# Performance work log

Measured on AMD Instinct MI355X. Metric: run time of the kernel, lower is better.

## Reference

```python
import jax, jax.numpy as jnp
import numpy as np

N = 50000   # nodes
E = 200000  # edges
C = 32      # conv_dim
ND = 75     # n_atom_features
ED = 12     # n_bond_features
L = 3       # num_layer
G = 500     # num graphs in batch
HID = 5     # neurons_message
EPS = 1e-5


def leaky(v):
    return jnp.where(v > 0, v, 0.01 * v)


def setup_inputs() -> dict:
    key = jax.random.key(0)
    ks = jax.random.split(key, 16)
    x = jax.random.normal(ks[0], (N, ND), jnp.float32)
    edge_index = jax.random.randint(ks[1], (2, E), 0, N, jnp.int32)
    edge_attr = jax.random.uniform(ks[2], (E, ED), jnp.float32)
    batch = jnp.sort(jax.random.randint(ks[3], (N,), 0, G, jnp.int32))
    return {
        "x": x,
        "edge_index": edge_index,
        "edge_attr": edge_attr,
        "batch": batch,
        "lin_W": jax.random.normal(ks[4], (ND, C), jnp.float32) * 0.1,
        "lin_b": jnp.zeros((C,), jnp.float32),
        "mes_W1": jax.random.normal(ks[5], (L, ED, HID), jnp.float32) * 0.3,
        "mes_b1": jnp.zeros((L, HID), jnp.float32),
        "mes_W2": jax.random.normal(ks[6], (L, HID, C * C), jnp.float32) * 0.05,
        "mes_b2": jnp.zeros((L, C * C), jnp.float32),
        "root_W": jax.random.normal(ks[7], (L, C, C), jnp.float32) * 0.1,
        "conv_b": jnp.zeros((L, C), jnp.float32),
        "bn_g": jnp.ones((L, C), jnp.float32),
        "bn_b": jnp.zeros((L, C), jnp.float32),
        "pred_W": jax.random.normal(ks[8], (C, 1), jnp.float32) * 0.1,
        "pred_b": jnp.zeros((1,), jnp.float32),
    }


def reference(x, edge_index, edge_attr, batch, lin_W, lin_b, mes_W1, mes_b1,
              mes_W2, mes_b2, root_W, conv_b, bn_g, bn_b, pred_W, pred_b):
    src, dst = edge_index[0], edge_index[1]
    # initial atom projection
    h = leaky(x @ lin_W + lin_b)  # [N, C]
    for l in range(L):
        # edge MLP -> per-edge weight matrix [E, C, C]
        w = jnp.maximum(edge_attr @ mes_W1[l] + mes_b1[l], 0.0)
        w = (w @ mes_W2[l] + mes_b2[l]).reshape(E, C, C)
        # gather source features, per-edge matmul, scatter-add to targets
        msg = jnp.einsum('ec,ecd->ed', h[src], w)  # [E, C]
        agg = jax.ops.segment_sum(msg, dst, num_segments=N)  # [N, C]
        out = agg + h @ root_W[l] + conv_b[l]
        # batch norm (batch statistics over nodes)
        mu = out.mean(axis=0)
        var = out.var(axis=0)
        out = (out - mu) / jnp.sqrt(var + EPS) * bn_g[l] + bn_b[l]
        if l < L - 1:
            out = leaky(out)
        h = out  # JK == 'last'
    # graph readout: scatter_add over batch ids, then prediction head
    g = jax.ops.segment_sum(h, batch, num_segments=G)  # [G, C]
    return g @ pred_W + pred_b  # [G, 1]
```

## Files before the change

kernel.cpp:

```cpp
#include <hip/hip_runtime.h>

namespace {

constexpr int kN = 50000, kE = 200000, kG = 500;
constexpr float kEps = 1e-5f;
constexpr int kNB = (kN + 255) / 256;

typedef short v8s __attribute__((ext_vector_type(8)));
typedef float v4f __attribute__((ext_vector_type(4)));

__device__ __forceinline__ unsigned short bf16rn(float x) {
    unsigned u = __float_as_uint(x);
    return (unsigned short)((u + 0x7FFFu + ((u >> 16) & 1u)) >> 16);
}
__device__ __forceinline__ float bf16lo(unsigned p) { return __uint_as_float(p << 16); }
__device__ __forceinline__ float bf16hi(unsigned p) { return __uint_as_float(p & 0xFFFF0000u); }
__device__ __forceinline__ unsigned pk2(float a, float b) {
    return (unsigned)bf16rn(a) | ((unsigned)bf16rn(b) << 16);
}

__global__ __launch_bounds__(256) void zero_init(int* __restrict__ deg,
                                                 float* __restrict__ stats) {
    int i = blockIdx.x * 256 + threadIdx.x;
    if (i < kN) deg[i] = 0;
    if (i < 1536) stats[i] = 0.f;
}

__global__ __launch_bounds__(256) void deg_hist(
    const int* __restrict__ ei, int* __restrict__ deg)
{
    int e = blockIdx.x * 256 + threadIdx.x;
    if (e < kE) atomicAdd(&deg[ei[kE + e]], 1);
}

__global__ __launch_bounds__(1024) void init_h(
    const float* __restrict__ x, const float* __restrict__ W,
    const float* __restrict__ b, float* __restrict__ hbuf)
{
    __shared__ unsigned short sx[256 * 96];
    __shared__ unsigned short sW[32 * 96];
    int t = threadIdx.x;
    for (int i = t; i < 256 * 96; i += 1024) sx[i] = 0;
    for (int i = t; i < 32 * 96; i += 1024) sW[i] = 0;
    __syncthreads();
    int tb = blockIdx.x * 256;
    int cnt = min(256, kN - tb);
    for (int i = t; i < cnt * 75; i += 1024) {
        int n = i / 75, f = i - n * 75;
        sx[n * 96 + f] = bf16rn(x[(size_t)tb * 75 + i]);
    }
    for (int i = t; i < 75 * 32; i += 1024) {
        int f = i >> 5, c = i & 31;
        sW[c * 96 + f] = bf16rn(W[i]);
    }
    __syncthreads();
    int l15 = t & 15, quad = (t >> 4) & 3, w = t >> 6;
    #pragma unroll
    for (int tile = 0; tile < 2; ++tile) {
        v4f acc = {0.f, 0.f, 0.f, 0.f};
        #pragma unroll
        for (int kc = 0; kc < 3; ++kc) {
            v8s a  = *(const v8s*)&sx[(w * 16 + l15) * 96 + kc * 32 + quad * 8];
            v8s bb = *(const v8s*)&sW[(tile * 16 + l15) * 96 + kc * 32 + quad * 8];
            acc = __builtin_amdgcn_mfma_f32_16x16x32_bf16(a, bb, acc, 0, 0, 0);
        }
        int c = tile * 16 + l15;
        float bc = b[c];
        #pragma unroll
        for (int r = 0; r < 4; ++r) {
            int n = tb + w * 16 + quad * 4 + r;
            if (n < kN) {
                float v = acc[r] + bc;
                hbuf[(size_t)n * 32 + c] = v > 0.f ? v : 0.01f * v;
            }
        }
    }
}

__global__ __launch_bounds__(256) void scan_part(
    const int* __restrict__ deg, int* __restrict__ blkSum)
{
    __shared__ int sc[256];
    int t = threadIdx.x;
    int idx = blockIdx.x * 256 + t;
    sc[t] = (idx < kN) ? deg[idx] : 0;
    __syncthreads();
    #pragma unroll
    for (int off = 128; off > 0; off >>= 1) {
        if (t < off) sc[t] += sc[t + off];
        __syncthreads();
    }
    if (t == 0) blkSum[blockIdx.x] = sc[0];
}

__global__ __launch_bounds__(256) void scan_top(
    const int* __restrict__ blkSum, int* __restrict__ blkOff,
    int* __restrict__ rowptr)
{
    __shared__ int sc[256];
    int t = threadIdx.x;
    int v = (t < kNB) ? blkSum[t] : 0;
    sc[t] = v;
    __syncthreads();
    #pragma unroll
    for (int off = 1; off < 256; off <<= 1) {
        int u = (t >= off) ? sc[t - off] : 0;
        __syncthreads();
        sc[t] += u;
        __syncthreads();
    }
    if (t < kNB) blkOff[t] = sc[t] - v;
    if (t == kNB - 1) rowptr[kN] = sc[t];
}

__global__ __launch_bounds__(256) void scan_add(
    const int* __restrict__ deg, const int* __restrict__ blkOff,
    int* __restrict__ rowptr, int* __restrict__ cursor)
{
    __shared__ int sc[256];
    int t = threadIdx.x;
    int idx = blockIdx.x * 256 + t;
    int v = (idx < kN) ? deg[idx] : 0;
    sc[t] = v;
    __syncthreads();
    #pragma unroll
    for (int off = 1; off < 256; off <<= 1) {
        int u = (t >= off) ? sc[t - off] : 0;
        __syncthreads();
        sc[t] += u;
        __syncthreads();
    }
    if (idx < kN) {
        int p = blkOff[blockIdx.x] + sc[t] - v;
        rowptr[idx] = p;
        cursor[idx] = p;
    }
}

__global__ __launch_bounds__(256) void hid_pre(
    const float* __restrict__ ea, const float* __restrict__ W1,
    const float* __restrict__ b1, const int* __restrict__ ei,
    int* __restrict__ cursor, uint4* __restrict__ hcsr)
{
    __shared__ float sE[256 * 13];
    __shared__ float sW[195];
    int t = threadIdx.x;
    for (int i = t; i < 195; i += 256) sW[i] = (i < 180) ? W1[i] : b1[i - 180];
    int base = blockIdx.x * 256;
    int cnt = min(256, kE - base);
    for (int i = t; i < cnt * 12; i += 256) {
        int el = i / 12, f = i - el * 12;
        sE[el * 13 + f] = ea[(size_t)base * 12 + i];
    }
    __syncthreads();
    if (t >= cnt) return;
    int e = base + t;
    int src = ei[e];
    int dst = ei[kE + e];
    int pos = atomicAdd(&cursor[dst], 1);
    float ef[12];
    #pragma unroll
    for (int j = 0; j < 12; ++j) ef[j] = sE[t * 13 + j];
    #pragma unroll
    for (int l = 0; l < 3; ++l) {
        float h[5];
        #pragma unroll
        for (int k = 0; k < 5; ++k) h[k] = sW[180 + l * 5 + k];
        #pragma unroll
        for (int f = 0; f < 12; ++f)
            #pragma unroll
            for (int k = 0; k < 5; ++k)
                h[k] = fmaf(ef[f], sW[l * 60 + f * 5 + k], h[k]);
        #pragma unroll
        for (int k = 0; k < 5; ++k) h[k] = h[k] > 0.f ? h[k] : 0.f;
        hcsr[(size_t)l * kE + pos] =
            make_uint4(pk2(h[0], h[1]), pk2(h[2], h[3]), pk2(h[4], 0.f),
                       (unsigned)src);
    }
}

__global__ __launch_bounds__(1024) void y_root(
    const float* __restrict__ hbuf, float* __restrict__ obuf,
    const float* __restrict__ W2, const float* __restrict__ b2,
    const float* __restrict__ rW, const float* __restrict__ convb,
    const float* __restrict__ statsR,
    const float* __restrict__ gPrev, const float* __restrict__ bPrev,
    int first, unsigned* __restrict__ Ydw)
{
    __shared__ unsigned short sh[256 * 32];
    __shared__ unsigned short sB[256 * 32];
    int t = threadIdx.x;
    int tb = blockIdx.x * 256;
    int cnt = min(256, kN - tb);
    for (int i = t; i < 8192; i += 1024) {
        int co = i >> 5, c = i & 31, d = co >> 3, k = co & 7;
        float v = (k < 5) ? W2[k * 1024 + c * 32 + d]
                : (k == 5) ? b2[c * 32 + d]
                : (k == 6) ? rW[c * 32 + d] : 0.f;
        sB[co * 32 + c] = bf16rn(v);
    }
    if (first) {
        #pragma unroll
        for (int j = 0; j < 8; ++j) {
            int idx = t + j * 1024;
            int nl = idx >> 5, c = idx & 31;
            float v = (nl < cnt) ? hbuf[(size_t)(tb + nl) * 32 + c] : 0.f;
            sh[idx] = bf16rn(v);
        }
    } else {
        int c = t & 31;
        float sum = 0.f, sq = 0.f;
        #pragma unroll
        for (int r = 0; r < 8; ++r) {
            sum += statsR[r * 64 + c];
            sq  += statsR[r * 64 + 32 + c];
        }
        float mu = sum * (1.f / kN);
        float var = sq * (1.f / kN) - mu * mu;
        float ivg = rsqrtf(var + kEps) * gPrev[c];
        float bb = bPrev[c];
        #pragma unroll
        for (int j = 0; j < 8; ++j) {
            int idx = t + j * 1024;
            int nl = idx >> 5;
            float v = 0.f;
            if (nl < cnt) {
                float o = obuf[(size_t)(tb + nl) * 32 + c];
                v = (o - mu) * ivg + bb;
                v = v > 0.f ? v : 0.01f * v;
            }
            sh[idx] = bf16rn(v);
        }
    }
    __syncthreads();
    int l15 = t & 15, quad = (t >> 4) & 3, w = t >> 6;
    int n = tb + w * 16 + l15;
    v8s bn_ = *(const v8s*)&sh[(w * 16 + l15) * 32 + quad * 8];
    #pragma unroll
    for (int i = 0; i < 16; ++i) {
        v8s a = *(const v8s*)&sB[(i * 16 + l15) * 32 + quad * 8];
        v4f acc = {0.f, 0.f, 0.f, 0.f};
        acc = __builtin_amdgcn_mfma_f32_16x16x32_bf16(a, bn_, acc, 0, 0, 0);
        if (n < kN) {
            int cb = i * 16 + quad * 4;
            int d = cb >> 3, koff = cb & 7;
            if (koff == 0) {
                Ydw[(size_t)n * 128 + d * 4]     = pk2(acc[0], acc[1]);
                Ydw[(size_t)n * 128 + d * 4 + 1] = pk2(acc[2], acc[3]);
            } else {
                Ydw[(size_t)n * 128 + d * 4 + 2] = pk2(acc[0], acc[1]);
                obuf[(size_t)n * 32 + d] = acc[2] + convb[d];
            }
        }
    }
}

__global__ __launch_bounds__(256) void agg(
    const int* __restrict__ rowptr, const uint4* __restrict__ hcsr,
    const unsigned short* __restrict__ Yus, float* __restrict__ obuf,
    float* __restrict__ statsR)
{
    int t = threadIdx.x;
    int grp = t >> 5, d = t & 31;
    int nbase = blockIdx.x * 16 + grp * 2;
    float s = 0.f, q = 0.f;
    #pragma unroll
    for (int ii = 0; ii < 2; ++ii) {
        int n = nbase + ii;
        if (n < kN) {
            float acc = obuf[(size_t)n * 32 + d];
            int j0 = rowptr[n], j1 = rowptr[n + 1];
            for (int j = j0; j < j1; ++j) {
                uint4 hq = hcsr[j];
                uint4 p = *(const uint4*)(Yus + (size_t)hq.w * 256 + d * 8);
                float m = bf16hi(p.z);
                m = fmaf(bf16lo(hq.x), bf16lo(p.x), m);
                m = fmaf(bf16hi(hq.x), bf16hi(p.x), m);
                m = fmaf(bf16lo(hq.y), bf16lo(p.y), m);
                m = fmaf(bf16hi(hq.y), bf16hi(p.y), m);
                m = fmaf(bf16lo(hq.z), bf16lo(p.z), m);
                acc += m;
            }
            obuf[(size_t)n * 32 + d] = acc;
            s += acc; q += acc * acc;
        }
    }
    __shared__ float ls[256];
    __shared__ float lq[256];
    ls[t] = s; lq[t] = q;
    __syncthreads();
    if (t < 128) { ls[t] += ls[t + 128]; lq[t] += lq[t + 128]; }
    __syncthreads();
    if (t < 64) { ls[t] += ls[t + 64]; lq[t] += lq[t + 64]; }
    __syncthreads();
    if (t < 32) {
        float* rep = statsR + (blockIdx.x & 7) * 64;
        atomicAdd(&rep[t], ls[t] + ls[t + 32]);
        atomicAdd(&rep[32 + t], lq[t] + lq[t + 32]);
    }
}

__global__ __launch_bounds__(256) void bn_norm_final(
    const float* __restrict__ obuf, const float* __restrict__ statsR,
    const float* __restrict__ g, const float* __restrict__ b,
    float* __restrict__ vbuf, const float* __restrict__ predW,
    float* __restrict__ out, const float* __restrict__ pred_b)
{
    int idx = blockIdx.x * 256 + threadIdx.x;
    if (idx < kG) out[idx] = pred_b[0];
    if (idx >= kN * 32) return;
    int c = idx & 31;
    float sum = 0.f, sq = 0.f;
    #pragma unroll
    for (int r = 0; r < 8; ++r) {
        sum += statsR[r * 64 + c];
        sq  += statsR[r * 64 + 32 + c];
    }
    float mu = sum * (1.f / kN);
    float var = sq * (1.f / kN) - mu * mu;
    float inv = rsqrtf(var + kEps);
    float v = (obuf[idx] - mu) * inv * g[c] + b[c];
    float pv = v * predW[c];
    #pragma unroll
    for (int off = 16; off > 0; off >>= 1) pv += __shfl_down(pv, off, 32);
    if (c == 0) vbuf[idx >> 5] = pv;
}

__global__ __launch_bounds__(256) void seg_readout(
    const float* __restrict__ vbuf, const int* __restrict__ batch,
    float* __restrict__ out)
{
    __shared__ float ls[kG];
    int t = threadIdx.x;
    for (int i = t; i < kG; i += 256) ls[i] = 0.f;
    __syncthreads();
    int base = blockIdx.x * 2048 + t * 8;
    int cur = -1; float acc = 0.f;
    #pragma unroll
    for (int i = 0; i < 8; ++i) {
        int n = base + i;
        if (n >= kN) break;
        int gi = batch[n];
        float val = vbuf[n];
        if (gi != cur) {
            if (cur >= 0) atomicAdd(&ls[cur], acc);
            cur = gi; acc = val;
        } else acc += val;
    }
    if (cur >= 0) atomicAdd(&ls[cur], acc);
    __syncthreads();
    for (int i = t; i < kG; i += 256) {
        float s = ls[i];
        if (s != 0.f) atomicAdd(&out[i], s);
    }
}

}

extern "C" void kernel_launch(void* const* d_in, const int* in_sizes, int n_in,
                              void* d_out, int out_size, void* d_ws, size_t ws_size,
                              hipStream_t stream)
{
    const float* x      = (const float*)d_in[0];
    const int*   ei     = (const int*)d_in[1];
    const float* ea     = (const float*)d_in[2];
    const int*   batch  = (const int*)d_in[3];
    const float* lin_W  = (const float*)d_in[4];
    const float* lin_b  = (const float*)d_in[5];
    const float* mes_W1 = (const float*)d_in[6];
    const float* mes_b1 = (const float*)d_in[7];
    const float* mes_W2 = (const float*)d_in[8];
    const float* mes_b2 = (const float*)d_in[9];
    const float* root_W = (const float*)d_in[10];
    const float* conv_b = (const float*)d_in[11];
    const float* bn_g   = (const float*)d_in[12];
    const float* bn_b   = (const float*)d_in[13];
    const float* pred_W = (const float*)d_in[14];
    const float* pred_b = (const float*)d_in[15];
    float* out = (float*)d_out;

    char* wsb = (char*)d_ws;
    float* stats   = (float*)wsb;
    int* deg       = (int*)(wsb + 8192);
    int* rowptr    = deg + kN;
    int* cursor    = rowptr + kN + 1;
    int* blkSum    = cursor + kN;
    int* blkOff    = blkSum + 256;
    float* hbuf    = (float*)(blkOff + 256);
    float* obuf    = hbuf + (size_t)kN * 32;
    unsigned short* Yus = (unsigned short*)(obuf + (size_t)kN * 32);
    unsigned* Ydw  = (unsigned*)Yus;
    uint4* hcsr    = (uint4*)(Yus + (size_t)kN * 256);
    float* vbuf    = (float*)Yus;

    zero_init<<<kNB, 256, 0, stream>>>(deg, stats);
    deg_hist<<<(kE + 255) / 256, 256, 0, stream>>>(ei, deg);
    init_h<<<kNB, 1024, 0, stream>>>(x, lin_W, lin_b, hbuf);
    scan_part<<<kNB, 256, 0, stream>>>(deg, blkSum);
    scan_top<<<1, 256, 0, stream>>>(blkSum, blkOff, rowptr);
    scan_add<<<kNB, 256, 0, stream>>>(deg, blkOff, rowptr, cursor);
    hid_pre<<<(kE + 255) / 256, 256, 0, stream>>>(ea, mes_W1, mes_b1, ei,
                                                  cursor, hcsr);

    for (int l = 0; l < 3; ++l) {
        y_root<<<kNB, 1024, 0, stream>>>(
            hbuf, obuf, mes_W2 + (size_t)l * 5120, mes_b2 + (size_t)l * 1024,
            root_W + (size_t)l * 1024, conv_b + l * 32,
            stats + (l ? (l - 1) * 512 : 0),
            bn_g + (l ? (l - 1) * 32 : 0), bn_b + (l ? (l - 1) * 32 : 0),
            l == 0 ? 1 : 0, Ydw);
        agg<<<(kN + 15) / 16, 256, 0, stream>>>(
            rowptr, hcsr + (size_t)l * kE, Yus, obuf, stats + l * 512);
    }

    bn_norm_final<<<(kN * 32 + 255) / 256, 256, 0, stream>>>(
        obuf, stats + 2 * 512, bn_g + 64, bn_b + 64, vbuf, pred_W, out, pred_b);
    seg_readout<<<(kN + 2047) / 2048, 256, 0, stream>>>(vbuf, batch, out);
}
```

Baseline: 306.3 us.

## Replace node-centric CSR aggregation with edge-parallel segmented atomic scatter plus BN reduce

Node-parallel CSR gather aggregation is replaced by an edge-parallel kernel. Each 32-lane group handles 16 dst-sorted edges, combines runs with the same destination and flushes them with float atomics into obuf. Batch-norm statistics now come from a separate reduction kernel, and rowptr is no longer built. The source index is packed into 16 bits next to h[4], which only holds if node ids stay below 65536. The change aims to fix load imbalance from variable node degree, at the cost of atomics, an extra pass over obuf, and nondeterministic summation order.

```diff
diff --git a/kernel.cpp b/kernel.cpp
--- a/kernel.cpp
+++ b/kernel.cpp
@@ -5,6 +5,7 @@
 constexpr int kN = 50000, kE = 200000, kG = 500;
 constexpr float kEps = 1e-5f;
 constexpr int kNB = (kN + 255) / 256;
+constexpr int kEB = (kE + 255) / 256;
 
 typedef short v8s __attribute__((ext_vector_type(8)));
 typedef float v4f __attribute__((ext_vector_type(4)));
@@ -94,8 +95,7 @@
 }
 
 __global__ __launch_bounds__(256) void scan_top(
-    const int* __restrict__ blkSum, int* __restrict__ blkOff,
-    int* __restrict__ rowptr)
+    const int* __restrict__ blkSum, int* __restrict__ blkOff)
 {
     __shared__ int sc[256];
     int t = threadIdx.x;
@@ -110,12 +110,11 @@
         __syncthreads();
     }
     if (t < kNB) blkOff[t] = sc[t] - v;
-    if (t == kNB - 1) rowptr[kN] = sc[t];
 }
 
 __global__ __launch_bounds__(256) void scan_add(
     const int* __restrict__ deg, const int* __restrict__ blkOff,
-    int* __restrict__ rowptr, int* __restrict__ cursor)
+    int* __restrict__ cursor)
 {
     __shared__ int sc[256];
     int t = threadIdx.x;
@@ -130,17 +129,13 @@
         sc[t] += u;
         __syncthreads();
     }
-    if (idx < kN) {
-        int p = blkOff[blockIdx.x] + sc[t] - v;
-        rowptr[idx] = p;
-        cursor[idx] = p;
-    }
+    if (idx < kN) cursor[idx] = blkOff[blockIdx.x] + sc[t] - v;
 }
 
 __global__ __launch_bounds__(256) void hid_pre(
     const float* __restrict__ ea, const float* __restrict__ W1,
     const float* __restrict__ b1, const int* __restrict__ ei,
-    int* __restrict__ cursor, uint4* __restrict__ hcsr)
+    int* __restrict__ cursor, uint4* __restrict__ hq)
 {
     __shared__ float sE[256 * 13];
     __shared__ float sW[195];
@@ -155,8 +150,8 @@
     __syncthreads();
     if (t >= cnt) return;
     int e = base + t;
-    int src = ei[e];
-    int dst = ei[kE + e];
+    unsigned src = (unsigned)ei[e];
+    unsigned dst = (unsigned)ei[kE + e];
     int pos = atomicAdd(&cursor[dst], 1);
     float ef[12];
     #pragma unroll
@@ -173,9 +168,9 @@
                 h[k] = fmaf(ef[f], sW[l * 60 + f * 5 + k], h[k]);
         #pragma unroll
         for (int k = 0; k < 5; ++k) h[k] = h[k] > 0.f ? h[k] : 0.f;
-        hcsr[(size_t)l * kE + pos] =
-            make_uint4(pk2(h[0], h[1]), pk2(h[2], h[3]), pk2(h[4], 0.f),
-                       (unsigned)src);
+        hq[(size_t)l * kE + pos] = make_uint4(
+            pk2(h[0], h[1]), pk2(h[2], h[3]),
+            (unsigned)bf16rn(h[4]) | (src << 16), dst);
     }
 }
 
@@ -255,38 +250,48 @@
     }
 }
 
-__global__ __launch_bounds__(256) void agg(
-    const int* __restrict__ rowptr, const uint4* __restrict__ hcsr,
-    const unsigned short* __restrict__ Yus, float* __restrict__ obuf,
-    float* __restrict__ statsR)
-{
-    int t = threadIdx.x;
-    int grp = t >> 5, d = t & 31;
-    int nbase = blockIdx.x * 16 + grp * 2;
-    float s = 0.f, q = 0.f;
-    #pragma unroll
-    for (int ii = 0; ii < 2; ++ii) {
-        int n = nbase + ii;
-        if (n < kN) {
-            float acc = obuf[(size_t)n * 32 + d];
-            int j0 = rowptr[n], j1 = rowptr[n + 1];
-            for (int j = j0; j < j1; ++j) {
-                uint4 hq = hcsr[j];
-                uint4 p = *(const uint4*)(Yus + (size_t)hq.w * 256 + d * 8);
-                float m = bf16hi(p.z);
-                m = fmaf(bf16lo(hq.x), bf16lo(p.x), m);
-                m = fmaf(bf16hi(hq.x), bf16hi(p.x), m);
-                m = fmaf(bf16lo(hq.y), bf16lo(p.y), m);
-                m = fmaf(bf16hi(hq.y), bf16hi(p.y), m);
-                m = fmaf(bf16lo(hq.z), bf16lo(p.z), m);
-                acc += m;
-            }
-            obuf[(size_t)n * 32 + d] = acc;
-            s += acc; q += acc * acc;
-        }
-    }
+__global__ __launch_bounds__(256) void edge_scat(
+    const uint4* __restrict__ hq, const unsigned short* __restrict__ Yus,
+    float* __restrict__ obuf)
+{
+    int gid = blockIdx.x * 256 + threadIdx.x;
+    int grp = gid >> 5;
+    if (grp >= kE / 16) return;
+    int d = gid & 31;
+    int e0 = grp * 16;
+    float acc = 0.f;
+    unsigned cur = 0xFFFFFFFFu;
+    #pragma unroll 4
+    for (int i = 0; i < 16; ++i) {
+        uint4 q = hq[e0 + i];
+        unsigned src = q.z >> 16;
+        uint4 p = *(const uint4*)(Yus + (size_t)src * 256 + d * 8);
+        float m = bf16hi(p.z);
+        m = fmaf(bf16lo(q.x), bf16lo(p.x), m);
+        m = fmaf(bf16hi(q.x), bf16hi(p.x), m);
+        m = fmaf(bf16lo(q.y), bf16lo(p.y), m);
+        m = fmaf(bf16hi(q.y), bf16hi(p.y), m);
+        m = fmaf(bf16lo(q.z), bf16lo(p.z), m);
+        if (q.w != cur) {
+            if (cur != 0xFFFFFFFFu) atomicAdd(&obuf[(size_t)cur * 32 + d], acc);
+            cur = q.w; acc = m;
+        } else acc += m;
+    }
+    if (cur != 0xFFFFFFFFu) atomicAdd(&obuf[(size_t)cur * 32 + d], acc);
+}
+
+__global__ __launch_bounds__(256) void bn_reduce(
+    const float* __restrict__ obuf, float* __restrict__ statsR)
+{
     __shared__ float ls[256];
     __shared__ float lq[256];
+    int t = threadIdx.x;
+    int c = t & 31, row = t >> 5;
+    float s = 0.f, q = 0.f;
+    for (int n = blockIdx.x * 8 + row; n < kN; n += gridDim.x * 8) {
+        float v = obuf[(size_t)n * 32 + c];
+        s += v; q += v * v;
+    }
     ls[t] = s; lq[t] = q;
     __syncthreads();
     if (t < 128) { ls[t] += ls[t + 128]; lq[t] += lq[t + 128]; }
@@ -380,28 +385,27 @@
     float* out = (float*)d_out;
 
     char* wsb = (char*)d_ws;
-    float* stats   = (float*)wsb;
-    int* deg       = (int*)(wsb + 8192);
-    int* rowptr    = deg + kN;
-    int* cursor    = rowptr + kN + 1;
-    int* blkSum    = cursor + kN;
-    int* blkOff    = blkSum + 256;
-    float* hbuf    = (float*)(blkOff + 256);
-    float* obuf    = hbuf + (size_t)kN * 32;
+    float* stats = (float*)wsb;
+    int* deg     = (int*)(wsb + 8192);
+    int* cursor  = deg + kN;
+    int* blkSum  = cursor + kN;
+    int* blkOff  = blkSum + 256;
+    float* hbuf  = (float*)(blkOff + 256);
+    float* obuf  = hbuf + (size_t)kN * 32;
     unsigned short* Yus = (unsigned short*)(obuf + (size_t)kN * 32);
-    unsigned* Ydw  = (unsigned*)Yus;
-    uint4* hcsr    = (uint4*)(Yus + (size_t)kN * 256);
-    float* vbuf    = (float*)Yus;
+    unsigned* Ydw = (unsigned*)Yus;
+    uint4* hq    = (uint4*)(Yus + (size_t)kN * 256);
+    float* vbuf  = (float*)Yus;
 
     zero_init<<<kNB, 256, 0, stream>>>(deg, stats);
-    deg_hist<<<(kE + 255) / 256, 256, 0, stream>>>(ei, deg);
+    deg_hist<<<kEB, 256, 0, stream>>>(ei, deg);
     init_h<<<kNB, 1024, 0, stream>>>(x, lin_W, lin_b, hbuf);
     scan_part<<<kNB, 256, 0, stream>>>(deg, blkSum);
-    scan_top<<<1, 256, 0, stream>>>(blkSum, blkOff, rowptr);
-    scan_add<<<kNB, 256, 0, stream>>>(deg, blkOff, rowptr, cursor);
-    hid_pre<<<(kE + 255) / 256, 256, 0, stream>>>(ea, mes_W1, mes_b1, ei,
-                                                  cursor, hcsr);
-
+    scan_top<<<1, 256, 0, stream>>>(blkSum, blkOff);
+    scan_add<<<kNB, 256, 0, stream>>>(deg, blkOff, cursor);
+    hid_pre<<<kEB, 256, 0, stream>>>(ea, mes_W1, mes_b1, ei, cursor, hq);
+
+    int scatBlocks = ((kE / 16) * 32 + 255) / 256;
     for (int l = 0; l < 3; ++l) {
         y_root<<<kNB, 1024, 0, stream>>>(
             hbuf, obuf, mes_W2 + (size_t)l * 5120, mes_b2 + (size_t)l * 1024,
@@ -409,8 +413,9 @@
             stats + (l ? (l - 1) * 512 : 0),
             bn_g + (l ? (l - 1) * 32 : 0), bn_b + (l ? (l - 1) * 32 : 0),
             l == 0 ? 1 : 0, Ydw);
-        agg<<<(kN + 15) / 16, 256, 0, stream>>>(
-            rowptr, hcsr + (size_t)l * kE, Yus, obuf, stats + l * 512);
+        edge_scat<<<scatBlocks, 256, 0, stream>>>(
+            hq + (size_t)l * kE, Yus, obuf);
+        bn_reduce<<<512, 256, 0, stream>>>(obuf, stats + l * 512);
     }
 
     bn_norm_final<<<(kN * 32 + 255) / 256, 256, 0, stream>>>(
```

Measured after the change: 289.7 us. 1.06x faster.
